# Performance work log

Hardware: AMD Instinct MI355X
Metric: run time of the kernel (lower is better)

Reference implementation:

```python
import jax, jax.numpy as jnp
import numpy as np

IN_F = 1024
OUT_F = 1024
GRID_SIZE = 8
GRID_LO, GRID_HI = -2.0, 2.0


def _grid_and_inv_denom():
    grid = jnp.linspace(GRID_LO, GRID_HI, GRID_SIZE)  # [G]
    inv_denom = 1.0 / (float((GRID_HI - GRID_LO) / (GRID_SIZE - 1)) + 1e-06)
    return grid, inv_denom


def setup_inputs() -> dict:
    key = jax.random.key(0)
    kx, kw, ks = jax.random.split(key, 3)
    x = jax.random.normal(kx, (4, 2048, IN_F), dtype=jnp.float32)
    # kaiming_uniform_(a=sqrt(5)) on [out,in]: bound = sqrt(6/((1+a^2)*fan_in)) = sqrt(1/fan_in)
    bound = float(np.sqrt(1.0 / IN_F))
    base_w = jax.random.uniform(kw, (OUT_F, IN_F), minval=-bound, maxval=bound, dtype=jnp.float32)
    base_b = jnp.zeros((OUT_F,), dtype=jnp.float32)
    spline_w = 0.02 * jax.random.normal(ks, (OUT_F, IN_F, GRID_SIZE), dtype=jnp.float32)
    return {"x": x, "base_w": base_w, "base_b": base_b, "spline_w": spline_w}


def reference(x, base_w, base_b, spline_w):
    grid, inv_denom = _grid_and_inv_denom()
    lead = x.shape[:-1]
    x_flat = x.reshape(-1, IN_F)  # [B, in]
    # base path: Linear(SiLU(x))
    base_out = jax.nn.silu(x_flat) @ base_w.T + base_b  # [B, out]
    # RBF basis expansion: [B, in, G]
    basis = jnp.exp(-(((x_flat[..., None] - grid) * inv_denom) ** 2))
    spline_out = jnp.einsum('big,oig->bo', basis, spline_w)  # [B, out]
    out = base_out + spline_out
    return out.reshape(*lead, OUT_F)
```

## Files before the change

kernel.cpp:

```cpp
#include <hip/hip_runtime.h>
#include <stdint.h>

namespace {

constexpr int IN_F = 1024;
constexpr int OUT_F = 1024;
constexpr int GSZ = 8;
constexpr int KTOT = IN_F + IN_F * GSZ;
constexpr int BK = 64;
constexpr int NT = KTOT / BK;
constexpr int NBASE = IN_F / BK;

constexpr int BM = 64, BN = 256;
constexpr int NBLK = OUT_F / BN;
constexpr size_t IMG_BYTES = (size_t)BN * BK * 2;
constexpr size_t WS_NEEDED = (size_t)NBLK * NT * IMG_BYTES;

constexpr double H_D     = 4.0 / 7.0;
constexpr double INVD_D  = 1.0 / (H_D + 1e-6);
constexpr double L2E_D   = 1.4426950408889634;
constexpr double SQL2E_D = 1.2011224087864498;
constexpr double CS_D    = INVD_D * SQL2E_D;
constexpr double DLT_D   = H_D * CS_D;

using short8 = __attribute__((ext_vector_type(8))) short;
using f32x4  = __attribute__((ext_vector_type(4))) float;

__device__ __forceinline__ unsigned cvt_pk(float lo, float hi) {
  unsigned r;
  asm("v_cvt_pk_bf16_f32 %0, %1, %2" : "=v"(r) : "v"(lo), "v"(hi));
  return r;
}
__device__ __forceinline__ float silu_f(float v) {
  float e = __builtin_amdgcn_exp2f(-v * (float)L2E_D);
  return v * __builtin_amdgcn_rcpf(1.0f + e);
}
__device__ __forceinline__ int swz(int row, int kk) {
  return (row * 128 + kk * 2) ^ ((row & 7) << 4);
}

__global__ void wprep(const float* __restrict__ bw, const float* __restrict__ sw,
                      char* __restrict__ wimg)
{
  const int total = NBLK * NT * BN * 8;
  for (int idx = blockIdx.x * blockDim.x + threadIdx.x; idx < total;
       idx += gridDim.x * blockDim.x) {
    const int kk8  = idx & 7;
    const int row  = (idx >> 3) & (BN - 1);
    const int rest = idx >> 11;
    const int step = rest % NT;
    const int nb   = rest / NT;
    const int o    = nb * BN + row;
    const int k    = step * BK + kk8 * 8;
    const float* src = (k < IN_F)
      ? (bw + (size_t)o * IN_F + k)
      : (sw + (size_t)o * (size_t)(IN_F * GSZ) + (k - IN_F));
    const float4 a = ((const float4*)src)[0];
    const float4 b = ((const float4*)src)[1];
    int4 v;
    v.x = (int)cvt_pk(a.x, a.y);
    v.y = (int)cvt_pk(a.z, a.w);
    v.z = (int)cvt_pk(b.x, b.y);
    v.w = (int)cvt_pk(b.z, b.w);
    *(int4*)(wimg + (size_t)rest * IMG_BYTES + swz(row, kk8 * 8)) = v;
  }
}

__global__ __launch_bounds__(256, 2)
void kan_fast(const float* __restrict__ x, const float* __restrict__ bb,
              const char* __restrict__ wimg, float* __restrict__ out)
{
  __shared__ char tA[2][BM * BK * 2];
  __shared__ char tB[2][BN * BK * 2];

  const int t    = threadIdx.x;
  const int lane = t & 63;
  const int wid  = t >> 6;
  const int wc   = wid * 64;
  const int bm0  = blockIdx.y * BM;
  const char* img = wimg + (size_t)blockIdx.x * NT * IMG_BYTES;
  const int bn0  = blockIdx.x * BN;

  const float CSf  = (float)CS_D;
  const float C0f  = (float)(-2.0 * CS_D);
  const float TDLT = (float)(2.0 * DLT_D);
  float Kc[7];
#pragma unroll
  for (int g = 0; g < 7; ++g) {
    const double cg  = (-2.0 + g * H_D) * CS_D;
    const double cg1 = (-2.0 + (g + 1) * H_D) * CS_D;
    Kc[g] = __builtin_amdgcn_exp2f((float)(-DLT_D * (cg + cg1)));
  }

  f32x4 acc[4][4];
#pragma unroll
  for (int m = 0; m < 4; ++m)
#pragma unroll
    for (int n = 0; n < 4; ++n) acc[m][n] = (f32x4)0.0f;

  float4 xE[4], xO[4];

  auto issue_B = [&](int step, char* dstB) {
    const char* g = img + (size_t)step * IMG_BYTES + t * 16;
    char* l = dstB + t * 16;
#pragma unroll
    for (int j = 0; j < 8; ++j)
      __builtin_amdgcn_global_load_lds(
        (const __attribute__((address_space(1))) void*)(g + j * 4096),
        (__attribute__((address_space(3))) void*)(l + j * 4096), 16, 0, 0);
  };

  auto load_x = [&](int step, float4 (&xr)[4]) {
    const int k0  = step * BK;
    const int row = t >> 2;
    if (k0 < IN_F) {
      const float* p = x + (size_t)(bm0 + row) * IN_F + k0 + (t & 3) * 16;
#pragma unroll
      for (int j = 0; j < 4; ++j) xr[j] = ((const float4*)p)[j];
    } else {
      const int i0 = (k0 - IN_F) >> 3;
      const float2 v = *(const float2*)(x + (size_t)(bm0 + row) * IN_F + i0 + (t & 3) * 2);
      xr[0].x = v.x; xr[0].y = v.y;
    }
  };

  auto conv_A = [&](int step, const float4 (&xr)[4], char* dstA) {
    const int row = t >> 2;
    if (step < NBASE) {
      unsigned q[8];
#pragma unroll
      for (int j = 0; j < 4; ++j) {
        q[2 * j]     = cvt_pk(silu_f(xr[j].x), silu_f(xr[j].y));
        q[2 * j + 1] = cvt_pk(silu_f(xr[j].z), silu_f(xr[j].w));
      }
      const int kc0 = (t & 3) * 16;
      *(int4*)(dstA + swz(row, kc0))     = make_int4(q[0], q[1], q[2], q[3]);
      *(int4*)(dstA + swz(row, kc0 + 8)) = make_int4(q[4], q[5], q[6], q[7]);
    } else {
      float2 xv; xv.x = xr[0].x; xv.y = xr[0].y;
      float2 tb; tb.x = xv.x * CSf;        tb.y = xv.y * CSf;
      float2 d0; d0.x = tb.x - C0f;        d0.y = tb.y - C0f;
      float2 e;
      e.x = __builtin_amdgcn_exp2f(-(d0.x * d0.x));
      e.y = __builtin_amdgcn_exp2f(-(d0.y * d0.y));
      float2 r;
      r.x = __builtin_amdgcn_exp2f(tb.x * TDLT);
      r.y = __builtin_amdgcn_exp2f(tb.y * TDLT);
      unsigned q0[4], q1[4];
#pragma unroll
      for (int g = 0; g < 4; ++g) {
        float2 a = e;
        float2 b;
        b.x = a.x * r.x * Kc[2 * g];
        b.y = a.y * r.y * Kc[2 * g];
        q0[g] = cvt_pk(a.x, b.x);
        q1[g] = cvt_pk(a.y, b.y);
        if (g < 3) {
          e.x = b.x * r.x * Kc[2 * g + 1];
          e.y = b.y * r.y * Kc[2 * g + 1];
        }
      }
      const int iloc = (t & 3) * 2;
      *(int4*)(dstA + swz(row, iloc * 8))       = make_int4(q0[0], q0[1], q0[2], q0[3]);
      *(int4*)(dstA + swz(row, (iloc + 1) * 8)) = make_int4(q1[0], q1[1], q1[2], q1[3]);
    }
  };

  auto read_frags = [&](const char* A, const char* B, int kh,
                        short8 (&af)[4], short8 (&bf)[4]) {
    const int r  = lane & 15;
    const int kq = (lane >> 4) * 8;
#pragma unroll
    for (int m = 0; m < 4; ++m)
      af[m] = *(const short8*)(A + swz(m * 16 + r, kh * 32 + kq));
#pragma unroll
    for (int n = 0; n < 4; ++n)
      bf[n] = *(const short8*)(B + swz(wc + n * 16 + r, kh * 32 + kq));
  };

  auto mfma16 = [&](short8 (&af)[4], short8 (&bf)[4]) {
#pragma unroll
    for (int m = 0; m < 4; ++m)
#pragma unroll
      for (int n = 0; n < 4; ++n)
        acc[m][n] = __builtin_amdgcn_mfma_f32_16x16x32_bf16(af[m], bf[n], acc[m][n], 0, 0, 0);
  };

  auto step_body = [&](int s, char* curA, char* curB, char* nxtA, char* nxtB,
                       const float4 (&xconv)[4], float4 (&xload)[4]) {
    short8 a0[4], b0[4], a1[4], b1[4];
    read_frags(curA, curB, 0, a0, b0);
    if (s + 1 < NT) issue_B(s + 1, nxtB);
    __builtin_amdgcn_sched_barrier(0);
    if (s + 2 < NT) load_x(s + 2, xload);
    if (s + 1 < NT) conv_A(s + 1, xconv, nxtA);
    __builtin_amdgcn_s_barrier();
    asm volatile("s_waitcnt lgkmcnt(0)" ::: "memory");
    __builtin_amdgcn_sched_barrier(0);
    __builtin_amdgcn_s_setprio(1);
    read_frags(curA, curB, 1, a1, b1);
    mfma16(a0, b0);
    asm volatile("s_waitcnt lgkmcnt(0)" ::: "memory");
    __builtin_amdgcn_sched_barrier(0);
    mfma16(a1, b1);
    __builtin_amdgcn_s_setprio(0);
    if (s + 2 < NT) {
      asm volatile("s_waitcnt vmcnt(1)" ::: "memory");
    } else {
      asm volatile("s_waitcnt vmcnt(0)" ::: "memory");
    }
    __builtin_amdgcn_s_barrier();
  };

  load_x(0, xE);
  load_x(1, xO);
  issue_B(0, tB[0]);
  conv_A(0, xE, tA[0]);
  __syncthreads();

  for (int s = 0; s < NT; s += 2) {
    step_body(s,     tA[0], tB[0], tA[1], tB[1], xO, xE);
    step_body(s + 1, tA[1], tB[1], tA[0], tB[0], xE, xO);
  }

  const int col = lane & 15;
  const int rr  = (lane >> 4) * 4;
#pragma unroll
  for (int m = 0; m < 4; ++m) {
    const int gr = bm0 + m * 16 + rr;
#pragma unroll
    for (int n = 0; n < 4; ++n) {
      const int gc = bn0 + wc + n * 16 + col;
      const float bias = bb[gc];
#pragma unroll
      for (int j = 0; j < 4; ++j)
        out[(size_t)(gr + j) * OUT_F + gc] = acc[m][n][j] + bias;
    }
  }
}

constexpr int SLDK = 64 + 8;

__device__ __forceinline__ unsigned f2bf(float f) {
  unsigned u = __float_as_uint(f);
  return (u + 0x7fffu + ((u >> 16) & 1u)) >> 16;
}
__device__ __forceinline__ unsigned pk2(float lo, float hi) {
  return f2bf(lo) | (f2bf(hi) << 16);
}

__global__ __launch_bounds__(256)
void kan_slow(const float* __restrict__ x, const float* __restrict__ bw,
              const float* __restrict__ bb, const float* __restrict__ sw,
              float* __restrict__ out)
{
  __shared__ unsigned short tA[128][SLDK];
  __shared__ unsigned short tB[128][SLDK];

  const int t    = threadIdx.x;
  const int lane = t & 63;
  const int wid  = t >> 6;
  const int wr   = (wid >> 1) * 64;
  const int wc   = (wid & 1) * 64;
  const int bm0  = blockIdx.x * 128;
  const int bn0  = blockIdx.y * 128;

  const float CS = (float)CS_D;
  float gsc[GSZ];
#pragma unroll
  for (int g = 0; g < GSZ; ++g)
    gsc[g] = (float)((-2.0 + g * H_D) * CS_D);

  f32x4 acc[4][4];
#pragma unroll
  for (int m = 0; m < 4; ++m)
#pragma unroll
    for (int n = 0; n < 4; ++n) acc[m][n] = (f32x4)0.0f;

  float4 rA[8], rB[8];
  const int rw = t >> 4;
  const int cw = (t & 15) * 4;

  auto load_tile = [&](int step) {
    const int k0 = step * BK;
    const bool base = (k0 < IN_F);
#pragma unroll
    for (int j = 0; j < 8; ++j) {
      const int row = j * 16 + rw;
      const float* p = base
        ? (bw + (size_t)(bn0 + row) * IN_F + k0 + cw)
        : (sw + (size_t)(bn0 + row) * (size_t)(IN_F * GSZ) + (k0 - IN_F) + cw);
      rB[j] = *(const float4*)p;
    }
    if (base) {
#pragma unroll
      for (int j = 0; j < 8; ++j) {
        const int row = j * 16 + rw;
        rA[j] = *(const float4*)(x + (size_t)(bm0 + row) * IN_F + k0 + cw);
      }
    } else {
      const int i0  = (k0 - IN_F) >> 3;
      const int row = t >> 1;
      rA[0] = *(const float4*)(x + (size_t)(bm0 + row) * IN_F + i0 + (t & 1) * 4);
    }
  };

  auto store_tile = [&](int step) {
    const int k0 = step * BK;
    const bool base = (k0 < IN_F);
#pragma unroll
    for (int j = 0; j < 8; ++j) {
      const int row = j * 16 + rw;
      uint2 v;
      v.x = pk2(rB[j].x, rB[j].y);
      v.y = pk2(rB[j].z, rB[j].w);
      *(uint2*)&tB[row][cw] = v;
    }
    if (base) {
#pragma unroll
      for (int j = 0; j < 8; ++j) {
        const int row = j * 16 + rw;
        uint2 v;
        v.x = pk2(silu_f(rA[j].x), silu_f(rA[j].y));
        v.y = pk2(silu_f(rA[j].z), silu_f(rA[j].w));
        *(uint2*)&tA[row][cw] = v;
      }
    } else {
      const int row  = t >> 1;
      const int half = t & 1;
      const float* xv = (const float*)&rA[0];
#pragma unroll
      for (int c = 0; c < 4; ++c) {
        const float tb = xv[c] * CS;
        union { unsigned u[4]; int4 v4; } pkv;
#pragma unroll
        for (int g = 0; g < 8; g += 2) {
          const float t0 = tb - gsc[g];
          const float t1 = tb - gsc[g + 1];
          const float e0 = __builtin_amdgcn_exp2f(-(t0 * t0));
          const float e1 = __builtin_amdgcn_exp2f(-(t1 * t1));
          pkv.u[g >> 1] = pk2(e0, e1);
        }
        const int kc = (half * 4 + c) * 8;
        *(int4*)&tA[row][kc] = pkv.v4;
      }
    }
  };

  auto compute_tile = [&]() {
    const int r  = lane & 15;
    const int kq = (lane >> 4) * 8;
#pragma unroll
    for (int kh = 0; kh < 2; ++kh) {
      short8 af[4], bf[4];
#pragma unroll
      for (int m = 0; m < 4; ++m)
        af[m] = *(const short8*)&tA[wr + m * 16 + r][kh * 32 + kq];
#pragma unroll
      for (int n = 0; n < 4; ++n)
        bf[n] = *(const short8*)&tB[wc + n * 16 + r][kh * 32 + kq];
#pragma unroll
      for (int m = 0; m < 4; ++m)
#pragma unroll
        for (int n = 0; n < 4; ++n)
          acc[m][n] = __builtin_amdgcn_mfma_f32_16x16x32_bf16(af[m], bf[n], acc[m][n], 0, 0, 0);
    }
  };

  load_tile(0);
  for (int step = 0; step < NT; ++step) {
    store_tile(step);
    __syncthreads();
    if (step + 1 < NT) load_tile(step + 1);
    compute_tile();
    __syncthreads();
  }

  const int col = lane & 15;
  const int rr  = (lane >> 4) * 4;
#pragma unroll
  for (int m = 0; m < 4; ++m) {
    const int gr = bm0 + wr + m * 16 + rr;
#pragma unroll
    for (int n = 0; n < 4; ++n) {
      const int gc = bn0 + wc + n * 16 + col;
      const float bias = bb[gc];
#pragma unroll
      for (int j = 0; j < 4; ++j)
        out[(size_t)(gr + j) * OUT_F + gc] = acc[m][n][j] + bias;
    }
  }
}

}

extern "C" void kernel_launch(void* const* d_in, const int* in_sizes, int n_in,
                              void* d_out, int out_size, void* d_ws, size_t ws_size,
                              hipStream_t stream) {
  const float *x, *bw, *bb, *sw;
  if (in_sizes[0] == OUT_F) {
    bb = (const float*)d_in[0];
    bw = (const float*)d_in[1];
    sw = (const float*)d_in[2];
    x  = (const float*)d_in[3];
  } else {
    x  = (const float*)d_in[0];
    bw = (const float*)d_in[1];
    bb = (const float*)d_in[2];
    sw = (const float*)d_in[3];
  }
  float* out = (float*)d_out;
  const int rows = (in_sizes[0] == OUT_F) ? in_sizes[3] / IN_F : in_sizes[0] / IN_F;

  if (ws_size >= WS_NEEDED && d_ws != nullptr && (rows % BM) == 0) {
    hipLaunchKernelGGL(wprep, dim3(2048), dim3(256), 0, stream, bw, sw, (char*)d_ws);
    dim3 grid(NBLK, rows / BM);
    hipLaunchKernelGGL(kan_fast, grid, dim3(256), 0, stream,
                       x, bb, (const char*)d_ws, out);
  } else {
    dim3 grid(rows / 128, OUT_F / 128);
    hipLaunchKernelGGL(kan_slow, grid, dim3(256), 0, stream, x, bw, bb, sw, out);
  }
}
```

Measured before the change: 202.9 us.

## Split 64x256 tile across eight waves instead of four

Doubles the block size of the fused KAN GEMM from 256 to 512 threads and arranges the waves as a 2x4 grid, so each wave computes a 32x64 sub-tile with half as many accumulators and A fragments. The A-tile conversion and B-tile async loads are redistributed so each thread handles half the elements. The aim is to raise the number of waves per CU and cut per-wave register pressure to better hide latency. The cost is that each B fragment is now read from LDS by two waves, and there are more barrier participants per step.

Result: no change. 206.8 us (+1.9%).

```diff
diff --git a/kernel.cpp b/kernel.cpp
--- a/kernel.cpp
+++ b/kernel.cpp
@@ -66,7 +66,7 @@
   }
 }
 
-__global__ __launch_bounds__(256, 2)
+__global__ __launch_bounds__(512, 4)
 void kan_fast(const float* __restrict__ x, const float* __restrict__ bb,
               const char* __restrict__ wimg, float* __restrict__ out)
 {
@@ -76,7 +76,8 @@
   const int t    = threadIdx.x;
   const int lane = t & 63;
   const int wid  = t >> 6;
-  const int wc   = wid * 64;
+  const int wr   = (wid >> 2) * 32;
+  const int wc   = (wid & 3) * 64;
   const int bm0  = blockIdx.y * BM;
   const char* img = wimg + (size_t)blockIdx.x * NT * IMG_BYTES;
   const int bn0  = blockIdx.x * BN;
@@ -92,103 +93,88 @@
     Kc[g] = __builtin_amdgcn_exp2f((float)(-DLT_D * (cg + cg1)));
   }
 
-  f32x4 acc[4][4];
-#pragma unroll
-  for (int m = 0; m < 4; ++m)
+  f32x4 acc[2][4];
+#pragma unroll
+  for (int m = 0; m < 2; ++m)
 #pragma unroll
     for (int n = 0; n < 4; ++n) acc[m][n] = (f32x4)0.0f;
 
-  float4 xE[4], xO[4];
+  float4 xE[2], xO[2];
+
+  const char* gB = img + wid * 4096 + lane * 16;
 
   auto issue_B = [&](int step, char* dstB) {
-    const char* g = img + (size_t)step * IMG_BYTES + t * 16;
-    char* l = dstB + t * 16;
-#pragma unroll
-    for (int j = 0; j < 8; ++j)
+    const char* g = gB + (size_t)step * IMG_BYTES;
+    char* l = dstB + wid * 4096;
+#pragma unroll
+    for (int j = 0; j < 4; ++j)
       __builtin_amdgcn_global_load_lds(
-        (const __attribute__((address_space(1))) void*)(g + j * 4096),
-        (__attribute__((address_space(3))) void*)(l + j * 4096), 16, 0, 0);
-  };
-
-  auto load_x = [&](int step, float4 (&xr)[4]) {
+        (const __attribute__((address_space(1))) void*)(g + j * 1024),
+        (__attribute__((address_space(3))) void*)(l + j * 1024), 16, 0, 0);
+  };
+
+  auto load_x = [&](int step, float4 (&xr)[2]) {
     const int k0  = step * BK;
-    const int row = t >> 2;
+    const int row = t >> 3;
     if (k0 < IN_F) {
-      const float* p = x + (size_t)(bm0 + row) * IN_F + k0 + (t & 3) * 16;
-#pragma unroll
-      for (int j = 0; j < 4; ++j) xr[j] = ((const float4*)p)[j];
+      const float* p = x + (size_t)(bm0 + row) * IN_F + k0 + (t & 7) * 8;
+      xr[0] = ((const float4*)p)[0];
+      xr[1] = ((const float4*)p)[1];
     } else {
       const int i0 = (k0 - IN_F) >> 3;
-      const float2 v = *(const float2*)(x + (size_t)(bm0 + row) * IN_F + i0 + (t & 3) * 2);
-      xr[0].x = v.x; xr[0].y = v.y;
-    }
-  };
-
-  auto conv_A = [&](int step, const float4 (&xr)[4], char* dstA) {
-    const int row = t >> 2;
+      xr[0].x = x[(size_t)(bm0 + row) * IN_F + i0 + (t & 7)];
+    }
+  };
+
+  auto conv_A = [&](int step, const float4 (&xr)[2], char* dstA) {
+    const int row = t >> 3;
+    char* dst = dstA + swz(row, (t & 7) * 8);
     if (step < NBASE) {
-      unsigned q[8];
-#pragma unroll
-      for (int j = 0; j < 4; ++j) {
-        q[2 * j]     = cvt_pk(silu_f(xr[j].x), silu_f(xr[j].y));
-        q[2 * j + 1] = cvt_pk(silu_f(xr[j].z), silu_f(xr[j].w));
+      unsigned q0 = cvt_pk(silu_f(xr[0].x), silu_f(xr[0].y));
+      unsigned q1 = cvt_pk(silu_f(xr[0].z), silu_f(xr[0].w));
+      unsigned q2 = cvt_pk(silu_f(xr[1].x), silu_f(xr[1].y));
+      unsigned q3 = cvt_pk(silu_f(xr[1].z), silu_f(xr[1].w));
+      *(int4*)dst = make_int4(q0, q1, q2, q3);
+    } else {
+      const float tb = xr[0].x * CSf;
+      const float d0 = tb - C0f;
+      float e = __builtin_amdgcn_exp2f(-(d0 * d0));
+      const float r = __builtin_amdgcn_exp2f(tb * TDLT);
+      unsigned q[4];
+#pragma unroll
+      for (int g = 0; g < 4; ++g) {
+        const float a = e;
+        const float b = a * r * Kc[2 * g];
+        q[g] = cvt_pk(a, b);
+        if (g < 3) e = b * r * Kc[2 * g + 1];
       }
-      const int kc0 = (t & 3) * 16;
-      *(int4*)(dstA + swz(row, kc0))     = make_int4(q[0], q[1], q[2], q[3]);
-      *(int4*)(dstA + swz(row, kc0 + 8)) = make_int4(q[4], q[5], q[6], q[7]);
-    } else {
-      float2 xv; xv.x = xr[0].x; xv.y = xr[0].y;
-      float2 tb; tb.x = xv.x * CSf;        tb.y = xv.y * CSf;
-      float2 d0; d0.x = tb.x - C0f;        d0.y = tb.y - C0f;
-      float2 e;
-      e.x = __builtin_amdgcn_exp2f(-(d0.x * d0.x));
-      e.y = __builtin_amdgcn_exp2f(-(d0.y * d0.y));
-      float2 r;
-      r.x = __builtin_amdgcn_exp2f(tb.x * TDLT);
-      r.y = __builtin_amdgcn_exp2f(tb.y * TDLT);
-      unsigned q0[4], q1[4];
-#pragma unroll
-      for (int g = 0; g < 4; ++g) {
-        float2 a = e;
-        float2 b;
-        b.x = a.x * r.x * Kc[2 * g];
-        b.y = a.y * r.y * Kc[2 * g];
-        q0[g] = cvt_pk(a.x, b.x);
-        q1[g] = cvt_pk(a.y, b.y);
-        if (g < 3) {
-          e.x = b.x * r.x * Kc[2 * g + 1];
-          e.y = b.y * r.y * Kc[2 * g + 1];
-        }
-      }
-      const int iloc = (t & 3) * 2;
-      *(int4*)(dstA + swz(row, iloc * 8))       = make_int4(q0[0], q0[1], q0[2], q0[3]);
-      *(int4*)(dstA + swz(row, (iloc + 1) * 8)) = make_int4(q1[0], q1[1], q1[2], q1[3]);
+      *(int4*)dst = make_int4(q[0], q[1], q[2], q[3]);
     }
   };
 
   auto read_frags = [&](const char* A, const char* B, int kh,
-                        short8 (&af)[4], short8 (&bf)[4]) {
+                        short8 (&af)[2], short8 (&bf)[4]) {
     const int r  = lane & 15;
     const int kq = (lane >> 4) * 8;
 #pragma unroll
-    for (int m = 0; m < 4; ++m)
-      af[m] = *(const short8*)(A + swz(m * 16 + r, kh * 32 + kq));
+    for (int m = 0; m < 2; ++m)
+      af[m] = *(const short8*)(A + swz(wr + m * 16 + r, kh * 32 + kq));
 #pragma unroll
     for (int n = 0; n < 4; ++n)
       bf[n] = *(const short8*)(B + swz(wc + n * 16 + r, kh * 32 + kq));
   };
 
-  auto mfma16 = [&](short8 (&af)[4], short8 (&bf)[4]) {
-#pragma unroll
-    for (int m = 0; m < 4; ++m)
+  auto mfma8 = [&](short8 (&af)[2], short8 (&bf)[4]) {
+#pragma unroll
+    for (int m = 0; m < 2; ++m)
 #pragma unroll
       for (int n = 0; n < 4; ++n)
         acc[m][n] = __builtin_amdgcn_mfma_f32_16x16x32_bf16(af[m], bf[n], acc[m][n], 0, 0, 0);
   };
 
   auto step_body = [&](int s, char* curA, char* curB, char* nxtA, char* nxtB,
-                       const float4 (&xconv)[4], float4 (&xload)[4]) {
-    short8 a0[4], b0[4], a1[4], b1[4];
+                       const float4 (&xconv)[2], float4 (&xload)[2]) {
+    short8 a0[2], b0[4], a1[2], b1[4];
     read_frags(curA, curB, 0, a0, b0);
     if (s + 1 < NT) issue_B(s + 1, nxtB);
     __builtin_amdgcn_sched_barrier(0);
@@ -199,10 +185,10 @@
     __builtin_amdgcn_sched_barrier(0);
     __builtin_amdgcn_s_setprio(1);
     read_frags(curA, curB, 1, a1, b1);
-    mfma16(a0, b0);
+    mfma8(a0, b0);
     asm volatile("s_waitcnt lgkmcnt(0)" ::: "memory");
     __builtin_amdgcn_sched_barrier(0);
-    mfma16(a1, b1);
+    mfma8(a1, b1);
     __builtin_amdgcn_s_setprio(0);
     if (s + 2 < NT) {
       asm volatile("s_waitcnt vmcnt(1)" ::: "memory");
@@ -226,8 +212,8 @@
   const int col = lane & 15;
   const int rr  = (lane >> 4) * 4;
 #pragma unroll
-  for (int m = 0; m < 4; ++m) {
-    const int gr = bm0 + m * 16 + rr;
+  for (int m = 0; m < 2; ++m) {
+    const int gr = bm0 + wr + m * 16 + rr;
 #pragma unroll
     for (int n = 0; n < 4; ++n) {
       const int gc = bn0 + wc + n * 16 + col;
@@ -415,7 +401,7 @@
   if (ws_size >= WS_NEEDED && d_ws != nullptr && (rows % BM) == 0) {
     hipLaunchKernelGGL(wprep, dim3(2048), dim3(256), 0, stream, bw, sw, (char*)d_ws);
     dim3 grid(NBLK, rows / BM);
-    hipLaunchKernelGGL(kan_fast, grid, dim3(256), 0, stream,
+    hipLaunchKernelGGL(kan_fast, grid, dim3(512), 0, stream,
                        x, bb, (const char*)d_ws, out);
   } else {
     dim3 grid(rows / 128, OUT_F / 128);
```
